# Kernel tuning notes

Hardware: AMD Instinct MI355X
Metric: run time of the kernel (lower is better)

## Reference

```python
import jax, jax.numpy as jnp
import numpy as np

TEMPERATURE = 0.1

def setup_inputs() -> dict:
    key = jax.random.key(0)
    k1, k2 = jax.random.split(key)
    A = jax.random.normal(k1, (16, 2048, 256), dtype=jnp.float32)
    B = jax.random.normal(k2, (16, 2048, 256), dtype=jnp.float32)
    return {"A": A, "B": B}

def _l2norm(x):
    # F.normalize(p=2, dim=-1): x / max(||x||, eps), eps=1e-12
    n = jnp.sqrt(jnp.sum(x * x, axis=-1, keepdims=True))
    return x / jnp.maximum(n, 1e-12)

def _nce_dir(sim):
    # sim: (B, N, N) logits; labels are the diagonal (row n -> col n)
    # mean over all B*N rows of (logsumexp(row) - row[label])
    lse = jax.nn.logsumexp(sim, axis=-1)            # (B, N)
    diag = jnp.diagonal(sim, axis1=-2, axis2=-1)    # (B, N)
    return jnp.mean(lse - diag)

def reference(A, B):
    emb1 = _l2norm(A)
    emb2 = _l2norm(B)
    sim12 = jnp.einsum("bnc,bmc->bnm", emb1, emb2) / TEMPERATURE  # (B, N, N)
    # sim21 is sim12 transposed per batch; reuse instead of a second bmm
    sim21 = jnp.swapaxes(sim12, -1, -2)
    return _nce_dir(sim12) + _nce_dir(sim21)
```

## Files before the change

kernel.cpp:

```cpp
#include <hip/hip_runtime.h>
#include <hip/hip_bf16.h>

typedef __attribute__((ext_vector_type(8))) __bf16 bf16x8;
typedef __attribute__((ext_vector_type(16))) float f32x16;

#define SCALE_L2E 14.4269504088896f
#define NTOT 32768

#define AS_GLOBAL __attribute__((address_space(1)))
#define AS_LDS    __attribute__((address_space(3)))

__device__ inline void async_copy16(const void* g, void* l) {
    __builtin_amdgcn_global_load_lds((const AS_GLOBAL void*)g, (AS_LDS void*)l, 16, 0, 0);
}

__device__ inline unsigned int f2bf(float f) {
    unsigned int u = __builtin_bit_cast(unsigned int, f);
    u += 0x7fffu + ((u >> 16) & 1u);
    return u >> 16;
}

__device__ inline uint4 pack8(float4 x, float4 y, float s) {
    uint4 r;
    r.x = f2bf(x.x * s) | (f2bf(x.y * s) << 16);
    r.y = f2bf(x.z * s) | (f2bf(x.w * s) << 16);
    r.z = f2bf(y.x * s) | (f2bf(y.y * s) << 16);
    r.w = f2bf(y.z * s) | (f2bf(y.w * s) << 16);
    return r;
}

__global__ __launch_bounds__(256) void nrm_kernel(
        const float* __restrict__ A, const float* __restrict__ B,
        uint4* __restrict__ E1, uint4* __restrict__ E2,
        float* __restrict__ diagPart) {
    __shared__ float sdiag;
    const int tid = threadIdx.x;
    if (tid == 0) sdiag = 0.f;
    __syncthreads();

    const int w = tid >> 6, l = tid & 63, q = l & 31, h = l >> 5;
    const int n0 = blockIdx.x * 8 + w * 2 + h;

    const float4* A4 = (const float4*)A + (size_t)n0 * 64 + q * 2;
    const float4* B4 = (const float4*)B + (size_t)n0 * 64 + q * 2;
    float4 a0 = A4[0], a1 = A4[1];
    float4 b0 = B4[0], b1 = B4[1];

    float sa = a0.x*a0.x + a0.y*a0.y + a0.z*a0.z + a0.w*a0.w
             + a1.x*a1.x + a1.y*a1.y + a1.z*a1.z + a1.w*a1.w;
    float sb = b0.x*b0.x + b0.y*b0.y + b0.z*b0.z + b0.w*b0.w
             + b1.x*b1.x + b1.y*b1.y + b1.z*b1.z + b1.w*b1.w;
    float dd = a0.x*b0.x + a0.y*b0.y + a0.z*b0.z + a0.w*b0.w
             + a1.x*b1.x + a1.y*b1.y + a1.z*b1.z + a1.w*b1.w;

    #pragma unroll
    for (int off = 1; off <= 16; off <<= 1) {
        sa += __shfl_xor(sa, off, 32);
        sb += __shfl_xor(sb, off, 32);
        dd += __shfl_xor(dd, off, 32);
    }
    const float ia = 1.0f / fmaxf(sqrtf(sa), 1e-12f);
    const float ib = 1.0f / fmaxf(sqrtf(sb), 1e-12f);
    if (q == 0) atomicAdd(&sdiag, dd * ia * ib * 10.0f);

    E1[(size_t)n0 * 32 + q] = pack8(a0, a1, ia);
    E2[(size_t)n0 * 32 + q] = pack8(b0, b1, ib);

    __syncthreads();
    if (tid == 0) diagPart[blockIdx.x] = sdiag;
}

__global__ __launch_bounds__(256, 4) void gemm_kernel(
        const bf16x8* __restrict__ E1, const bf16x8* __restrict__ E2,
        float* __restrict__ colSum, float* __restrict__ rowSum) {
    __shared__ bf16x8 Bbuf[2][1024];
    __shared__ float colLDS[2048];

    const int tid = threadIdx.x, w = tid >> 6, l = tid & 63;
    const int m = l & 31, ko = l >> 5;
    const int rt = blockIdx.x, ct = blockIdx.y, b = blockIdx.z;

    for (int i = l; i < 512; i += 64) colLDS[w * 512 + i] = 0.f;

    const bf16x8* Arow = E1 + ((size_t)b * 2048 + rt * 128 + w * 32 + m) * 32 + ko;
    bf16x8 af[16];
    #pragma unroll
    for (int kt = 0; kt < 16; ++kt) af[kt] = Arow[kt * 2];

    float rowAcc[16];
    #pragma unroll
    for (int r = 0; r < 16; ++r) rowAcc[r] = 0.f;

    const bf16x8* Brow = E2 + ((size_t)b * 2048 + ct * 512 + m) * 32 + ko;

    auto stage = [&](int buf, int cg) {
        const bf16x8* src = Brow + (size_t)cg * 32 * 32 + (w * 4) * 2;
        #pragma unroll
        for (int j = 0; j < 4; ++j)
            async_copy16(src + j * 2, &Bbuf[buf][(w * 4 + j) * 64]);
    };

    stage(0, 0);
    __syncthreads();

    for (int cg = 0; cg < 16; ++cg) {
        if (cg < 15) stage((cg + 1) & 1, cg + 1);

        const bf16x8* Bf = Bbuf[cg & 1];
        f32x16 acc;
        #pragma unroll
        for (int r = 0; r < 16; ++r) acc[r] = 0.f;

        #pragma unroll
        for (int kt = 0; kt < 16; ++kt)
            acc = __builtin_amdgcn_mfma_f32_32x32x16_bf16(af[kt], Bf[kt * 64 + l], acc, 0, 0, 0);

        float p = 0.f;
        #pragma unroll
        for (int r = 0; r < 16; ++r) {
            float e = exp2f(fmaf(acc[r], SCALE_L2E, -SCALE_L2E));
            rowAcc[r] += e;
            p += e;
        }
        p += __shfl_xor(p, 32);
        if (l < 32) colLDS[w * 512 + cg * 32 + l] += p;
        __syncthreads();
    }

    #pragma unroll
    for (int r = 0; r < 16; ++r) {
        #pragma unroll
        for (int off = 1; off <= 16; off <<= 1)
            rowAcc[r] += __shfl_xor(rowAcc[r], off);
    }
    if ((l & 31) == 0) {
        float* rs = rowSum + (size_t)b * 2048 + rt * 128 + w * 32 + 4 * (l >> 5);
        #pragma unroll
        for (int r = 0; r < 16; ++r)
            atomicAdd(&rs[(r & 3) + 8 * (r >> 2)], rowAcc[r]);
    }

    float* gcol = colSum + (size_t)b * 2048 + ct * 512;
    for (int i = tid; i < 512; i += 256) {
        float s = colLDS[i] + colLDS[512 + i] + colLDS[1024 + i] + colLDS[1536 + i];
        atomicAdd(&gcol[i], s);
    }
}

__global__ __launch_bounds__(256) void fin1_kernel(
        const float* __restrict__ red, float* __restrict__ scalars) {
    const int tid = threadIdx.x;
    float s = 0.f;
    #pragma unroll
    for (int k = 0; k < 4; ++k)
        s += logf(red[blockIdx.x * 1024 + k * 256 + tid]);
    #pragma unroll
    for (int off = 1; off <= 32; off <<= 1) s += __shfl_xor(s, off);
    __shared__ float part[4];
    if ((tid & 63) == 0) part[tid >> 6] = s;
    __syncthreads();
    if (tid == 0)
        atomicAdd(&scalars[0], part[0] + part[1] + part[2] + part[3]);
}

__global__ __launch_bounds__(256) void fin2_kernel(
        const float* __restrict__ diagPart, const float* __restrict__ scalars,
        float* __restrict__ out) {
    const int tid = threadIdx.x;
    float d = 0.f;
    for (int i = tid; i < 4096; i += 256) d += diagPart[i];
    #pragma unroll
    for (int off = 1; off <= 32; off <<= 1) d += __shfl_xor(d, off);
    __shared__ float part[4];
    if ((tid & 63) == 0) part[tid >> 6] = d;
    __syncthreads();
    if (tid == 0) {
        const float diag = part[0] + part[1] + part[2] + part[3];
        out[0] = (scalars[0] - 2.0f * diag) / (float)NTOT + 20.0f;
    }
}

extern "C" void kernel_launch(void* const* d_in, const int* in_sizes, int n_in,
                              void* d_out, int out_size, void* d_ws, size_t ws_size,
                              hipStream_t stream) {
    const float* A = (const float*)d_in[0];
    const float* B = (const float*)d_in[1];

    char* w = (char*)d_ws;
    uint4* E1 = (uint4*)w;
    uint4* E2 = (uint4*)(w + (size_t)16 * 1024 * 1024);
    float* colSum = (float*)(w + (size_t)32 * 1024 * 1024);
    float* rowSum = colSum + NTOT;
    float* scalars = rowSum + NTOT;
    float* diagPart = scalars + 2;

    hipMemsetAsync(colSum, 0, (size_t)(2 * NTOT + 2) * 4, stream);

    hipLaunchKernelGGL(nrm_kernel, dim3(4096), dim3(256), 0, stream,
                       A, B, E1, E2, diagPart);
    hipLaunchKernelGGL(gemm_kernel, dim3(16, 4, 16), dim3(256), 0, stream,
                       (const bf16x8*)E1, (const bf16x8*)E2, colSum, rowSum);
    hipLaunchKernelGGL(fin1_kernel, dim3(64), dim3(256), 0, stream,
                       colSum, scalars);
    hipLaunchKernelGGL(fin2_kernel, dim3(1), dim3(256), 0, stream,
                       diagPart, scalars, (float*)d_out);
}
```

Measured before the change: 161.0 us.

## Store embeddings in MFMA fragment order and double row tile per wave

The normalization kernel now handles four row pairs per wave with software-prefetched loads, and writes bf16 embeddings in a pre-swizzled fragment layout so the GEMM loads fragments contiguously. Each GEMM wave now computes two 32-row MFMA tiles that share each B fragment, halving the grid and the B staging traffic per output. The cost is more registers per wave (launch bounds dropped to 2 blocks per CU) and fewer blocks, which may reduce latency hiding. The diag partial count is adjusted to match the smaller normalization grid.

```diff
diff --git a/kernel.cpp b/kernel.cpp
--- a/kernel.cpp
+++ b/kernel.cpp
@@ -29,75 +29,94 @@
     return r;
 }
 
+__device__ inline float sum8(float4 x, float4 y) {
+    return x.x + x.y + x.z + x.w + y.x + y.y + y.z + y.w;
+}
+__device__ inline float dot8(float4 x, float4 y) {
+    return x.x*y.x + x.y*y.y + x.z*y.z + x.w*y.w;
+}
+
 __global__ __launch_bounds__(256) void nrm_kernel(
         const float* __restrict__ A, const float* __restrict__ B,
-        uint4* __restrict__ E1, uint4* __restrict__ E2,
+        uint4* __restrict__ E1f, uint4* __restrict__ E2f,
         float* __restrict__ diagPart) {
-    __shared__ float sdiag;
-    const int tid = threadIdx.x;
-    if (tid == 0) sdiag = 0.f;
-    __syncthreads();
-
-    const int w = tid >> 6, l = tid & 63, q = l & 31, h = l >> 5;
-    const int n0 = blockIdx.x * 8 + w * 2 + h;
-
-    const float4* A4 = (const float4*)A + (size_t)n0 * 64 + q * 2;
-    const float4* B4 = (const float4*)B + (size_t)n0 * 64 + q * 2;
-    float4 a0 = A4[0], a1 = A4[1];
-    float4 b0 = B4[0], b1 = B4[1];
-
-    float sa = a0.x*a0.x + a0.y*a0.y + a0.z*a0.z + a0.w*a0.w
-             + a1.x*a1.x + a1.y*a1.y + a1.z*a1.z + a1.w*a1.w;
-    float sb = b0.x*b0.x + b0.y*b0.y + b0.z*b0.z + b0.w*b0.w
-             + b1.x*b1.x + b1.y*b1.y + b1.z*b1.z + b1.w*b1.w;
-    float dd = a0.x*b0.x + a0.y*b0.y + a0.z*b0.z + a0.w*b0.w
-             + a1.x*b1.x + a1.y*b1.y + a1.z*b1.z + a1.w*b1.w;
-
-    #pragma unroll
-    for (int off = 1; off <= 16; off <<= 1) {
-        sa += __shfl_xor(sa, off, 32);
-        sb += __shfl_xor(sb, off, 32);
-        dd += __shfl_xor(dd, off, 32);
-    }
-    const float ia = 1.0f / fmaxf(sqrtf(sa), 1e-12f);
-    const float ib = 1.0f / fmaxf(sqrtf(sb), 1e-12f);
-    if (q == 0) atomicAdd(&sdiag, dd * ia * ib * 10.0f);
-
-    E1[(size_t)n0 * 32 + q] = pack8(a0, a1, ia);
-    E2[(size_t)n0 * 32 + q] = pack8(b0, b1, ib);
-
-    __syncthreads();
-    if (tid == 0) diagPart[blockIdx.x] = sdiag;
-}
-
-__global__ __launch_bounds__(256, 4) void gemm_kernel(
-        const bf16x8* __restrict__ E1, const bf16x8* __restrict__ E2,
+    const int tid = threadIdx.x, w = tid >> 6, l = tid & 63;
+    const int q = l & 31, h = l >> 5;
+    const int wid = blockIdx.x * 4 + w;
+
+    const float4* A4 = (const float4*)A + ((size_t)wid * 8 + h) * 64 + q * 2;
+    const float4* B4 = (const float4*)B + ((size_t)wid * 8 + h) * 64 + q * 2;
+
+    float ddAcc = 0.f;
+    float4 a0 = A4[0], a1 = A4[1], b0 = B4[0], b1 = B4[1];
+
+    #pragma unroll
+    for (int i = 0; i < 4; ++i) {
+        float4 na0, na1, nb0, nb1;
+        if (i < 3) {
+            const float4* An = A4 + (i + 1) * 128;
+            const float4* Bn = B4 + (i + 1) * 128;
+            na0 = An[0]; na1 = An[1]; nb0 = Bn[0]; nb1 = Bn[1];
+        }
+        float sa = dot8(a0, a0) + dot8(a1, a1);
+        float sb = dot8(b0, b0) + dot8(b1, b1);
+        float dd = dot8(a0, b0) + dot8(a1, b1);
+        #pragma unroll
+        for (int off = 1; off <= 16; off <<= 1) {
+            sa += __shfl_xor(sa, off);
+            sb += __shfl_xor(sb, off);
+            dd += __shfl_xor(dd, off);
+        }
+        const float ia = 1.0f / fmaxf(sqrtf(sa), 1e-12f);
+        const float ib = 1.0f / fmaxf(sqrtf(sb), 1e-12f);
+        if (q == 0) ddAcc += dd * ia * ib * 10.0f;
+
+        const int n0 = wid * 8 + i * 2 + h;
+        const size_t chunk = (size_t)(n0 >> 11) * 65536
+                           + (size_t)((n0 & 2047) >> 5) * 1024
+                           + (q >> 1) * 64 + (q & 1) * 32 + (n0 & 31);
+        E1f[chunk] = pack8(a0, a1, ia);
+        E2f[chunk] = pack8(b0, b1, ib);
+
+        a0 = na0; a1 = na1; b0 = nb0; b1 = nb1;
+    }
+
+    #pragma unroll
+    for (int off = 1; off <= 32; off <<= 1) ddAcc += __shfl_xor(ddAcc, off);
+    __shared__ float part[4];
+    if (l == 0) part[w] = ddAcc;
+    __syncthreads();
+    if (tid == 0) diagPart[blockIdx.x] = part[0] + part[1] + part[2] + part[3];
+}
+
+__global__ __launch_bounds__(256, 2) void gemm_kernel(
+        const bf16x8* __restrict__ E1f, const uint4* __restrict__ E2f,
         float* __restrict__ colSum, float* __restrict__ rowSum) {
     __shared__ bf16x8 Bbuf[2][1024];
     __shared__ float colLDS[2048];
 
     const int tid = threadIdx.x, w = tid >> 6, l = tid & 63;
-    const int m = l & 31, ko = l >> 5;
     const int rt = blockIdx.x, ct = blockIdx.y, b = blockIdx.z;
 
     for (int i = l; i < 512; i += 64) colLDS[w * 512 + i] = 0.f;
 
-    const bf16x8* Arow = E1 + ((size_t)b * 2048 + rt * 128 + w * 32 + m) * 32 + ko;
-    bf16x8 af[16];
-    #pragma unroll
-    for (int kt = 0; kt < 16; ++kt) af[kt] = Arow[kt * 2];
-
-    float rowAcc[16];
-    #pragma unroll
-    for (int r = 0; r < 16; ++r) rowAcc[r] = 0.f;
-
-    const bf16x8* Brow = E2 + ((size_t)b * 2048 + ct * 512 + m) * 32 + ko;
+    const bf16x8* Af0 = E1f + (size_t)b * 65536 + (size_t)(rt * 8 + w * 2) * 1024 + l;
+    const bf16x8* Af1 = Af0 + 1024;
+    bf16x8 af0[16], af1[16];
+    #pragma unroll
+    for (int kt = 0; kt < 16; ++kt) { af0[kt] = Af0[kt * 64]; af1[kt] = Af1[kt * 64]; }
+
+    float rowAcc0[16], rowAcc1[16];
+    #pragma unroll
+    for (int r = 0; r < 16; ++r) { rowAcc0[r] = 0.f; rowAcc1[r] = 0.f; }
+
+    const uint4* Bb = E2f + (size_t)b * 65536 + (size_t)ct * 16384 + l;
 
     auto stage = [&](int buf, int cg) {
-        const bf16x8* src = Brow + (size_t)cg * 32 * 32 + (w * 4) * 2;
+        const uint4* src = Bb + (size_t)cg * 1024 + (w * 4) * 64;
         #pragma unroll
         for (int j = 0; j < 4; ++j)
-            async_copy16(src + j * 2, &Bbuf[buf][(w * 4 + j) * 64]);
+            async_copy16(src + j * 64, &Bbuf[buf][(w * 4 + j) * 64]);
     };
 
     stage(0, 0);
@@ -107,20 +126,25 @@
         if (cg < 15) stage((cg + 1) & 1, cg + 1);
 
         const bf16x8* Bf = Bbuf[cg & 1];
-        f32x16 acc;
-        #pragma unroll
-        for (int r = 0; r < 16; ++r) acc[r] = 0.f;
-
-        #pragma unroll
-        for (int kt = 0; kt < 16; ++kt)
-            acc = __builtin_amdgcn_mfma_f32_32x32x16_bf16(af[kt], Bf[kt * 64 + l], acc, 0, 0, 0);
+        f32x16 acc0, acc1;
+        #pragma unroll
+        for (int r = 0; r < 16; ++r) { acc0[r] = 0.f; acc1[r] = 0.f; }
+
+        #pragma unroll
+        for (int kt = 0; kt < 16; ++kt) {
+            bf16x8 bfrag = Bf[kt * 64 + l];
+            acc0 = __builtin_amdgcn_mfma_f32_32x32x16_bf16(af0[kt], bfrag, acc0, 0, 0, 0);
+            acc1 = __builtin_amdgcn_mfma_f32_32x32x16_bf16(af1[kt], bfrag, acc1, 0, 0, 0);
+        }
 
         float p = 0.f;
         #pragma unroll
         for (int r = 0; r < 16; ++r) {
-            float e = exp2f(fmaf(acc[r], SCALE_L2E, -SCALE_L2E));
-            rowAcc[r] += e;
-            p += e;
+            float e0 = exp2f(fmaf(acc0[r], SCALE_L2E, -SCALE_L2E));
+            float e1 = exp2f(fmaf(acc1[r], SCALE_L2E, -SCALE_L2E));
+            rowAcc0[r] += e0;
+            rowAcc1[r] += e1;
+            p += e0 + e1;
         }
         p += __shfl_xor(p, 32);
         if (l < 32) colLDS[w * 512 + cg * 32 + l] += p;
@@ -130,14 +154,19 @@
     #pragma unroll
     for (int r = 0; r < 16; ++r) {
         #pragma unroll
-        for (int off = 1; off <= 16; off <<= 1)
-            rowAcc[r] += __shfl_xor(rowAcc[r], off);
+        for (int off = 1; off <= 16; off <<= 1) {
+            rowAcc0[r] += __shfl_xor(rowAcc0[r], off);
+            rowAcc1[r] += __shfl_xor(rowAcc1[r], off);
+        }
     }
     if ((l & 31) == 0) {
-        float* rs = rowSum + (size_t)b * 2048 + rt * 128 + w * 32 + 4 * (l >> 5);
-        #pragma unroll
-        for (int r = 0; r < 16; ++r)
-            atomicAdd(&rs[(r & 3) + 8 * (r >> 2)], rowAcc[r]);
+        float* rs = rowSum + (size_t)b * 2048 + rt * 256 + w * 64 + 4 * (l >> 5);
+        #pragma unroll
+        for (int r = 0; r < 16; ++r) {
+            const int rl = (r & 3) + 8 * (r >> 2);
+            atomicAdd(&rs[rl], rowAcc0[r]);
+            atomicAdd(&rs[rl + 32], rowAcc1[r]);
+        }
     }
 
     float* gcol = colSum + (size_t)b * 2048 + ct * 512;
@@ -168,7 +197,7 @@
         float* __restrict__ out) {
     const int tid = threadIdx.x;
     float d = 0.f;
-    for (int i = tid; i < 4096; i += 256) d += diagPart[i];
+    for (int i = tid; i < 1024; i += 256) d += diagPart[i];
     #pragma unroll
     for (int off = 1; off <= 32; off <<= 1) d += __shfl_xor(d, off);
     __shared__ float part[4];
@@ -187,8 +216,8 @@
     const float* B = (const float*)d_in[1];
 
     char* w = (char*)d_ws;
-    uint4* E1 = (uint4*)w;
-    uint4* E2 = (uint4*)(w + (size_t)16 * 1024 * 1024);
+    uint4* E1f = (uint4*)w;
+    uint4* E2f = (uint4*)(w + (size_t)16 * 1024 * 1024);
     float* colSum = (float*)(w + (size_t)32 * 1024 * 1024);
     float* rowSum = colSum + NTOT;
     float* scalars = rowSum + NTOT;
@@ -196,10 +225,10 @@
 
     hipMemsetAsync(colSum, 0, (size_t)(2 * NTOT + 2) * 4, stream);
 
-    hipLaunchKernelGGL(nrm_kernel, dim3(4096), dim3(256), 0, stream,
-                       A, B, E1, E2, diagPart);
-    hipLaunchKernelGGL(gemm_kernel, dim3(16, 4, 16), dim3(256), 0, stream,
-                       (const bf16x8*)E1, (const bf16x8*)E2, colSum, rowSum);
+    hipLaunchKernelGGL(nrm_kernel, dim3(1024), dim3(256), 0, stream,
+                       A, B, E1f, E2f, diagPart);
+    hipLaunchKernelGGL(gemm_kernel, dim3(8, 4, 16), dim3(256), 0, stream,
+                       (const bf16x8*)E1f, (const uint4*)E2f, colSum, rowSum);
     hipLaunchKernelGGL(fin1_kernel, dim3(64), dim3(256), 0, stream,
                        colSum, scalars);
     hipLaunchKernelGGL(fin2_kernel, dim3(1), dim3(256), 0, stream,
```

Measured after the change: 160.4 us. No clear change (-0.4%).
